# Performance work log

Hardware: AMD Instinct MI355X
Metric: run time of the kernel (lower is better)

Reference implementation:

```python
import jax, jax.numpy as jnp
import numpy as np

# ---- CRF hyperparameters (init_kwargs) ----
NUM_CLASSES = 4
RADIUS = 10            # guided filter radius -> 21x21 kernel
EPS = 1e-4
THETA_GAMMA = 2.5
G_RADIUS = int(THETA_GAMMA * 4)  # gaussian layer radius = 10 -> 21x21 kernel
SPATIAL_COMPAT = 3.0
BILATERAL_COMPAT = 10.0
NUM_ITERATIONS = 5
RGB_W = np.array([0.2989, 0.5870, 0.1140], dtype=np.float32)  # tf rgb_to_grayscale


def _make_kernel(radius, theta):
    x, y = np.mgrid[-radius:radius + 1, -radius:radius + 1]
    k = np.exp(-(x ** 2 + y ** 2) / (2.0 * theta ** 2))
    k = k / k.sum()
    k[radius, radius] = 0.0  # zero out center (no self-message)
    return jnp.asarray(k, dtype=jnp.float32)

_GAUSS_K = _make_kernel(G_RADIUS, THETA_GAMMA)          # spatial gaussian kernel
_GUIDED_K = _make_kernel(RADIUS, RADIUS / 3.0)          # guided-filter gaussian kernel


def _depthwise(src, k2d, r):
    # src: [B,H,W,C], k2d: [kh,kw]; zero-padded depthwise conv (same as pad+VALID)
    c = src.shape[-1]
    kh, kw = k2d.shape
    k = jnp.broadcast_to(k2d[:, :, None, None], (kh, kw, 1, c))
    return jax.lax.conv_general_dilated(
        src, k, window_strides=(1, 1), padding=[(r, r), (r, r)],
        dimension_numbers=('NHWC', 'HWIO', 'NHWC'), feature_group_count=c)


def _gaussian(src):
    return _depthwise(src, _GAUSS_K, G_RADIUS)


def _guided(gray, p):
    # guided gaussian filter with single-channel guide `gray` [B,H,W,1]
    gf = lambda s: _depthwise(s, _GUIDED_K, RADIUS)
    mean_I = gf(gray)                       # [B,H,W,1]
    mean_p = gf(p)                          # [B,H,W,C]
    mean_Ip = gf(gray * p)
    cov_Ip = mean_Ip - mean_I * mean_p
    mean_II = gf(gray * gray)
    var_I = mean_II - mean_I * mean_I
    a = cov_Ip / (var_I + EPS)
    b = mean_p - a * mean_I
    return gf(a) * gray + gf(b)


def setup_inputs() -> dict:
    key = jax.random.key(0)
    k1, k2 = jax.random.split(key)
    unary = jax.random.normal(k1, (1, 512, 512, NUM_CLASSES), dtype=jnp.float32)
    image = jax.random.uniform(k2, (1, 512, 512, 3), dtype=jnp.float32)
    return {"unary": unary, "image": image}


def reference(unary, image):
    gray = (image @ jnp.asarray(RGB_W))[..., None]        # [B,H,W,1]
    ones = jnp.ones_like(unary)
    spatial_norm = _gaussian(ones)
    bilateral_norm = _guided(gray, ones)

    Q = jax.nn.softmax(-unary, axis=-1)
    for _ in range(NUM_ITERATIONS):
        spatial_out = _gaussian(Q) / spatial_norm
        bilateral_out = _guided(gray, Q) / bilateral_norm
        # spatial_weights = SPATIAL_COMPAT*I, bilateral_weights = BILATERAL_COMPAT*I,
        # compatibility = -I  => matmuls reduce to scalar scaling + negation
        message = SPATIAL_COMPAT * spatial_out + BILATERAL_COMPAT * bilateral_out
        pairwise = -message
        Q = jax.nn.softmax(-unary - pairwise, axis=-1)
    return Q
```

## Files before the change

### kernel.cpp

```cpp
#include <hip/hip_runtime.h>
#include <hip/hip_cooperative_groups.h>
#include <hip/hip_fp16.h>
#include <math.h>

namespace cg = cooperative_groups;

#define W 512
#define H 512
#define NPIX (W*H)
#define RAD 10
#define KS 21
#define CRF_EPS 1e-4f

#define TX 32
#define TY 8
#define CIN (TX + 2*RAD)
#define RIN (TY + 2*RAD)
#define GX (W / TX)
#define GY (H / TY)
#define NBLK (GX*GY)
#define NVT (CIN * 4)

#define SM_BYTES 29952
#define OFF_R1 23296

struct W21 { float w[KS]; };

struct Params {
    const float4* unary;
    const float*  image;
    unsigned short* grayh;
    ushort4* Qh;
    float2*  a1b1;
    ushort4* ah;
    ushort4* bh;
    float4*  Qfinal;
    W21 wg, wu;
    float c0g, c0u;
};

__device__ __forceinline__ float4 f4(float x, float y, float z, float w_) {
    return make_float4(x, y, z, w_);
}
__device__ __forceinline__ float4 fma4(float s, float4 a, float4 acc) {
    acc.x = fmaf(s, a.x, acc.x); acc.y = fmaf(s, a.y, acc.y);
    acc.z = fmaf(s, a.z, acc.z); acc.w = fmaf(s, a.w, acc.w);
    return acc;
}
__device__ __forceinline__ int swz(int b, int N) {
    return (b & 7) * (N >> 3) + (b >> 3);
}
__device__ __forceinline__ ushort4 pack4(float4 v) {
    ushort4 r;
    r.x = __half_as_ushort(__float2half_rn(v.x));
    r.y = __half_as_ushort(__float2half_rn(v.y));
    r.z = __half_as_ushort(__float2half_rn(v.z));
    r.w = __half_as_ushort(__float2half_rn(v.w));
    return r;
}
__device__ __forceinline__ float4 unpack4(ushort4 v) {
    return f4(__half2float(__ushort_as_half(v.x)),
              __half2float(__ushort_as_half(v.y)),
              __half2float(__ushort_as_half(v.z)),
              __half2float(__ushort_as_half(v.w)));
}
__device__ __forceinline__ unsigned short packh(float v) {
    return __half_as_ushort(__float2half_rn(v));
}
__device__ __forceinline__ float unpackh(unsigned short v) {
    return __half2float(__ushort_as_half(v));
}


__global__ __launch_bounds__(256, 5) void k_crf(Params P) {
    cg::grid_group grid = cg::this_grid();
    __shared__ __align__(16) char smem[SM_BYTES];
    float4* sQ  = (float4*)smem;
    float2* s2t = (float2*)smem;
    float2* ii0 = (float2*)smem;
    float*  sG  = (float*)(smem + OFF_R1);
    float2* ii1 = (float2*)(smem + OFF_R1);
    float4* i0  = (float4*)smem;
    float4* i1  = (float4*)(smem + 6656);
    float4* i2  = (float4*)(smem + OFF_R1);
    float4* ia  = (float4*)(smem + OFF_R1);
    float4* ib  = (float4*)smem;

    int t = threadIdx.x;
    int L = swz(blockIdx.x, NBLK);
    int x0 = (L & (GX - 1)) * TX, y0 = (L >> 4) * TY;
    int row = t >> 5, col = t & 31;
    int py = y0 + row, px = x0 + col;
    int p = py * W + px;
    int vc = t % CIN, vr0 = (t / CIN) * 2;
    int cidx = (row + RAD) * CIN + col + RAD;

    {
        int pi = blockIdx.x * 256 + t;
        float r = P.image[3 * pi], g = P.image[3 * pi + 1], b = P.image[3 * pi + 2];
        P.grayh[pi] = packh(0.2989f * r + 0.5870f * g + 0.1140f * b);
        float4 u0 = P.unary[pi];
        float mn = fminf(fminf(u0.x, u0.y), fminf(u0.z, u0.w));
        float ex = expf(mn - u0.x), ey = expf(mn - u0.y);
        float ez = expf(mn - u0.z), ew = expf(mn - u0.w);
        float inv = 1.f / (ex + ey + ez + ew);
        P.Qh[pi] = pack4(f4(ex * inv, ey * inv, ez * inv, ew * inv));
    }
    float4 u = P.unary[p];
    float Sgx = 0.f, Sgy = 0.f, Sux = 0.f, Suy = 0.f;
    #pragma unroll
    for (int d = -RAD; d <= RAD; ++d) {
        int xx = px + d, yy = py + d;
        if (xx >= 0 && xx < W) { Sgx += P.wg.w[d + RAD]; Sux += P.wu.w[d + RAD]; }
        if (yy >= 0 && yy < H) { Sgy += P.wg.w[d + RAD]; Suy += P.wu.w[d + RAD]; }
    }
    float s3 = 3.f / (Sgx * Sgy - P.c0g);
    grid.sync();

    for (int i = t; i < RIN * CIN; i += 256) {
        int r = i / CIN, c = i - r * CIN;
        int gx = x0 + c - RAD, gy = y0 + r - RAD;
        float g = 0.f;
        if ((unsigned)gx < W && (unsigned)gy < H) g = unpackh(P.grayh[gy * W + gx]);
        sG[i] = g;
    }
    __syncthreads();
    if (t < NVT) {
        float2 acc0 = make_float2(0.f, 0.f), acc1 = acc0;
        #pragma unroll
        for (int s = 0; s < 22; ++s) {
            float g = sG[(vr0 + s) * CIN + vc];
            if (s <= 20) { float wgv = P.wu.w[s] * g; acc0.x += wgv; acc0.y = fmaf(wgv, g, acc0.y); }
            if (s >= 1)  { float wgv = P.wu.w[s-1] * g; acc1.x += wgv; acc1.y = fmaf(wgv, g, acc1.y); }
        }
        ii0[vr0 * CIN + vc] = acc0;
        ii0[(vr0 + 1) * CIN + vc] = acc1;
    }
    __syncthreads();
    float gv = sG[cidx];
    float mI, iv, ibn;
    {
        float2 A = make_float2(0.f, 0.f);
        #pragma unroll
        for (int d = 0; d < KS; ++d) {
            float2 v = ii0[row * CIN + col + d];
            A.x = fmaf(P.wu.w[d], v.x, A.x);
            A.y = fmaf(P.wu.w[d], v.y, A.y);
        }
        mI = A.x - P.c0u * gv;
        float mII = A.y - P.c0u * gv * gv;
        iv = 1.f / ((mII - mI * mI) + CRF_EPS);
        float N = Sux * Suy - P.c0u;
        float a1v = mI * (1.f - N) * iv;
        float b1v = N - a1v * mI;
        P.a1b1[p] = make_float2(a1v, b1v);
    }
    grid.sync();

    for (int i = t; i < RIN * CIN; i += 256) {
        int r = i / CIN, c = i - r * CIN;
        int gx = x0 + c - RAD, gy = y0 + r - RAD;
        float2 v = make_float2(0.f, 0.f);
        if ((unsigned)gx < W && (unsigned)gy < H) v = P.a1b1[gy * W + gx];
        s2t[i] = v;
    }
    __syncthreads();
    if (t < NVT) {
        float2 acc0 = make_float2(0.f, 0.f), acc1 = acc0;
        #pragma unroll
        for (int s = 0; s < 22; ++s) {
            float2 v = s2t[(vr0 + s) * CIN + vc];
            if (s <= 20) { acc0.x = fmaf(P.wu.w[s], v.x, acc0.x); acc0.y = fmaf(P.wu.w[s], v.y, acc0.y); }
            if (s >= 1)  { acc1.x = fmaf(P.wu.w[s-1], v.x, acc1.x); acc1.y = fmaf(P.wu.w[s-1], v.y, acc1.y); }
        }
        ii1[vr0 * CIN + vc] = acc0;
        ii1[(vr0 + 1) * CIN + vc] = acc1;
    }
    __syncthreads();
    {
        float2 A = make_float2(0.f, 0.f);
        #pragma unroll
        for (int d = 0; d < KS; ++d) {
            float2 v = ii1[row * CIN + col + d];
            A.x = fmaf(P.wu.w[d], v.x, A.x);
            A.y = fmaf(P.wu.w[d], v.y, A.y);
        }
        float2 cen = s2t[cidx];
        float va = A.x - P.c0u * cen.x;
        float vb = A.y - P.c0u * cen.y;
        ibn = 10.f / (va * gv + vb);
    }

    float px_part, py_part, pz_part, pw_part;
    for (int it = 0; it < 5; ++it) {
        __syncthreads();
        for (int i = t; i < RIN * CIN; i += 256) {
            int r = i / CIN, c = i - r * CIN;
            int gx = x0 + c - RAD, gy = y0 + r - RAD;
            float4 q = f4(0.f, 0.f, 0.f, 0.f); float g = 0.f;
            if ((unsigned)gx < W && (unsigned)gy < H) {
                int pp = gy * W + gx;
                q = unpack4(P.Qh[pp]); g = unpackh(P.grayh[pp]);
            }
            sQ[i] = q; sG[i] = g;
        }
        __syncthreads();
        float4 Qc = sQ[cidx];
        float4 a0[2], a1r[2], a2[2];
        if (t < NVT) {
            #pragma unroll
            for (int j = 0; j < 2; ++j) { a0[j] = f4(0,0,0,0); a1r[j] = a0[j]; a2[j] = a0[j]; }
            #pragma unroll
            for (int s = 0; s < 22; ++s) {
                float4 q = sQ[(vr0 + s) * CIN + vc];
                float g = sG[(vr0 + s) * CIN + vc];
                float4 gq = f4(g * q.x, g * q.y, g * q.z, g * q.w);
                if (s <= 20) {
                    a0[0]  = fma4(P.wg.w[s], q, a0[0]);
                    a1r[0] = fma4(P.wu.w[s], q, a1r[0]);
                    a2[0]  = fma4(P.wu.w[s], gq, a2[0]);
                }
                if (s >= 1) {
                    a0[1]  = fma4(P.wg.w[s-1], q, a0[1]);
                    a1r[1] = fma4(P.wu.w[s-1], q, a1r[1]);
                    a2[1]  = fma4(P.wu.w[s-1], gq, a2[1]);
                }
            }
        }
        __syncthreads();
        if (t < NVT) {
            #pragma unroll
            for (int j = 0; j < 2; ++j) {
                i0[(vr0 + j) * CIN + vc] = a0[j];
                i1[(vr0 + j) * CIN + vc] = a1r[j];
                i2[(vr0 + j) * CIN + vc] = a2[j];
            }
        }
        __syncthreads();
        {
            float4 A0 = f4(0,0,0,0), A1 = A0, A2 = A0;
            #pragma unroll
            for (int d = 0; d < KS; ++d) {
                A0 = fma4(P.wg.w[d], i0[row * CIN + col + d], A0);
                A1 = fma4(P.wu.w[d], i1[row * CIN + col + d], A1);
                A2 = fma4(P.wu.w[d], i2[row * CIN + col + d], A2);
            }
            float4 g4  = fma4(-P.c0g, Qc, A0);
            float4 m4  = fma4(-P.c0u, Qc, A1);
            float4 mi4 = fma4(-P.c0u * gv, Qc, A2);
            float4 a, b;
            a.x = (mi4.x - mI * m4.x) * iv; a.y = (mi4.y - mI * m4.y) * iv;
            a.z = (mi4.z - mI * m4.z) * iv; a.w = (mi4.w - mI * m4.w) * iv;
            b.x = m4.x - a.x * mI; b.y = m4.y - a.y * mI;
            b.z = m4.z - a.z * mI; b.w = m4.w - a.w * mI;
            px_part = fmaf(s3, g4.x, -u.x); py_part = fmaf(s3, g4.y, -u.y);
            pz_part = fmaf(s3, g4.z, -u.z); pw_part = fmaf(s3, g4.w, -u.w);
            P.ah[p] = pack4(a); P.bh[p] = pack4(b);
        }
        grid.sync();

        for (int i = t; i < RIN * CIN; i += 256) {
            int r = i / CIN, c = i - r * CIN;
            int gx = x0 + c - RAD, gy = y0 + r - RAD;
            float4 v = f4(0.f, 0.f, 0.f, 0.f);
            if ((unsigned)gx < W && (unsigned)gy < H) v = unpack4(P.ah[gy * W + gx]);
            sQ[i] = v;
        }
        __syncthreads();
        float4 Ac = sQ[cidx];
        if (t < NVT) {
            float4 va0 = f4(0,0,0,0), va1 = va0;
            #pragma unroll
            for (int s = 0; s < 22; ++s) {
                float4 v = sQ[(vr0 + s) * CIN + vc];
                if (s <= 20) va0 = fma4(P.wu.w[s], v, va0);
                if (s >= 1)  va1 = fma4(P.wu.w[s-1], v, va1);
            }
            ia[vr0 * CIN + vc] = va0;
            ia[(vr0 + 1) * CIN + vc] = va1;
        }
        __syncthreads();
        for (int i = t; i < RIN * CIN; i += 256) {
            int r = i / CIN, c = i - r * CIN;
            int gx = x0 + c - RAD, gy = y0 + r - RAD;
            float4 v = f4(0.f, 0.f, 0.f, 0.f);
            if ((unsigned)gx < W && (unsigned)gy < H) v = unpack4(P.bh[gy * W + gx]);
            sQ[i] = v;
        }
        __syncthreads();
        float4 Bc = sQ[cidx];
        float4 vb0 = f4(0,0,0,0), vb1 = vb0;
        if (t < NVT) {
            #pragma unroll
            for (int s = 0; s < 22; ++s) {
                float4 v = sQ[(vr0 + s) * CIN + vc];
                if (s <= 20) vb0 = fma4(P.wu.w[s], v, vb0);
                if (s >= 1)  vb1 = fma4(P.wu.w[s-1], v, vb1);
            }
        }
        __syncthreads();
        if (t < NVT) {
            ib[vr0 * CIN + vc] = vb0;
            ib[(vr0 + 1) * CIN + vc] = vb1;
        }
        __syncthreads();
        {
            float4 VA = f4(0,0,0,0), VB = VA;
            #pragma unroll
            for (int d = 0; d < KS; ++d) {
                VA = fma4(P.wu.w[d], ia[row * CIN + col + d], VA);
                VB = fma4(P.wu.w[d], ib[row * CIN + col + d], VB);
            }
            float4 a4 = fma4(-P.c0u, Ac, VA);
            float4 b4 = fma4(-P.c0u, Bc, VB);
            float lx = fmaf(fmaf(a4.x, gv, b4.x), ibn, px_part);
            float ly = fmaf(fmaf(a4.y, gv, b4.y), ibn, py_part);
            float lz = fmaf(fmaf(a4.z, gv, b4.z), ibn, pz_part);
            float lw = fmaf(fmaf(a4.w, gv, b4.w), ibn, pw_part);
            float m = fmaxf(fmaxf(lx, ly), fmaxf(lz, lw));
            float ex = expf(lx - m), ey = expf(ly - m);
            float ez = expf(lz - m), ew = expf(lw - m);
            float inv = 1.f / (ex + ey + ez + ew);
            float4 qn = f4(ex * inv, ey * inv, ez * inv, ew * inv);
            if (it == 4) P.Qfinal[p] = qn;
            else         P.Qh[p] = pack4(qn);
        }
        if (it < 4) grid.sync();
    }
}


__global__ __launch_bounds__(256) void fb_init(const float* __restrict__ img,
        const float4* __restrict__ unary, unsigned short* __restrict__ grayh,
        ushort4* __restrict__ Qh, float* __restrict__ Sg, float* __restrict__ Su,
        W21 wg, W21 wu) {
    int t = threadIdx.x;
    if (blockIdx.x < 2) {
        int x = blockIdx.x * 256 + t;
        float sg = 0.f, su = 0.f;
        #pragma unroll
        for (int d = -RAD; d <= RAD; ++d) {
            int xx = x + d;
            if (xx >= 0 && xx < W) { sg += wg.w[d + RAD]; su += wu.w[d + RAD]; }
        }
        Sg[x] = sg; Su[x] = su;
    }
    int b = swz(blockIdx.x, NPIX / 256);
    int p = b * 256 + t;
    float r = img[3 * p], g = img[3 * p + 1], bch = img[3 * p + 2];
    grayh[p] = packh(0.2989f * r + 0.5870f * g + 0.1140f * bch);
    float4 u = unary[p];
    float mn = fminf(fminf(u.x, u.y), fminf(u.z, u.w));
    float ex = expf(mn - u.x), ey = expf(mn - u.y), ez = expf(mn - u.z), ew = expf(mn - u.w);
    float inv = 1.f / (ex + ey + ez + ew);
    Qh[p] = pack4(f4(ex * inv, ey * inv, ez * inv, ew * inv));
}

__global__ __launch_bounds__(256, 4) void fb_s1(const unsigned short* __restrict__ grayh,
        const float* __restrict__ Su, float* __restrict__ mean_I,
        float* __restrict__ inv_var, float2* __restrict__ a1b1,
        W21 wu, float c0u) {
    __shared__ float  sg[RIN][CIN];
    __shared__ float2 ii[TY][CIN];
    int L = swz(blockIdx.x, NBLK);
    int x0 = (L & (GX - 1)) * TX, y0 = (L >> 4) * TY;
    int t = threadIdx.x;
    for (int i = t; i < RIN * CIN; i += 256) {
        int r = i / CIN, c = i - r * CIN;
        int gx = x0 + c - RAD, gy = y0 + r - RAD;
        float g = 0.f;
        if ((unsigned)gx < W && (unsigned)gy < H) g = unpackh(grayh[gy * W + gx]);
        sg[r][c] = g;
    }
    __syncthreads();
    if (t < NVT) {
        int c = t % CIN, r0 = (t / CIN) * 2;
        float2 acc0 = make_float2(0.f, 0.f), acc1 = acc0;
        #pragma unroll
        for (int s = 0; s < 22; ++s) {
            float g = sg[r0 + s][c];
            if (s <= 20) { float wgv = wu.w[s] * g; acc0.x += wgv; acc0.y = fmaf(wgv, g, acc0.y); }
            if (s >= 1)  { float wgv = wu.w[s-1] * g; acc1.x += wgv; acc1.y = fmaf(wgv, g, acc1.y); }
        }
        ii[r0][c] = acc0; ii[r0 + 1][c] = acc1;
    }
    __syncthreads();
    int row = t >> 5, col = t & 31;
    float2 A = make_float2(0.f, 0.f);
    #pragma unroll
    for (int d = 0; d < KS; ++d) {
        float2 v = ii[row][col + d];
        A.x = fmaf(wu.w[d], v.x, A.x);
        A.y = fmaf(wu.w[d], v.y, A.y);
    }
    int py = y0 + row, px = x0 + col;
    int p = py * W + px;
    float gc = sg[row + RAD][col + RAD];
    float mI = A.x - c0u * gc;
    float mII = A.y - c0u * gc * gc;
    float iv = 1.f / ((mII - mI * mI) + CRF_EPS);
    float N = Su[px] * Su[py] - c0u;
    float av = mI * (1.f - N) * iv;
    float bv = N - av * mI;
    mean_I[p] = mI; inv_var[p] = iv; a1b1[p] = make_float2(av, bv);
}

__global__ __launch_bounds__(256, 4) void fb_s2(const float2* __restrict__ a1b1,
        const unsigned short* __restrict__ grayh, float* __restrict__ inv_bn,
        W21 wu, float c0u) {
    __shared__ float2 s2[RIN][CIN];
// ... 144 lines not shown
    for (int i = t; i < RIN * CIN; i += 256) {
        int r = i / CIN, c = i - r * CIN;
        int gx = x0 + c - RAD, gy = y0 + r - RAD;
        float4 v = f4(0.f, 0.f, 0.f, 0.f);
        if ((unsigned)gx < W && (unsigned)gy < H) v = unpack4(A[gy * W + gx]);
        sT[i] = v;
    }
    __syncthreads();
    float4 Ac = sT[(row + RAD) * CIN + col + RAD];
    float4 va0 = f4(0,0,0,0), va1 = va0;
    if (t < NVT) {
        #pragma unroll
        for (int s = 0; s < 22; ++s) {
            float4 v = sT[(vr0 + s) * CIN + vc];
            if (s <= 20) va0 = fma4(wu.w[s], v, va0);
            if (s >= 1)  va1 = fma4(wu.w[s-1], v, va1);
        }
        ia[vr0 * CIN + vc] = va0;
        ia[(vr0 + 1) * CIN + vc] = va1;
    }
    __syncthreads();
    for (int i = t; i < RIN * CIN; i += 256) {
        int r = i / CIN, c = i - r * CIN;
        int gx = x0 + c - RAD, gy = y0 + r - RAD;
        float4 v = f4(0.f, 0.f, 0.f, 0.f);
        if ((unsigned)gx < W && (unsigned)gy < H) v = unpack4(B[gy * W + gx]);
        sT[i] = v;
    }
    __syncthreads();
    float4 Bc = sT[(row + RAD) * CIN + col + RAD];
    float4 vb0 = f4(0,0,0,0), vb1 = vb0;
    if (t < NVT) {
        #pragma unroll
        for (int s = 0; s < 22; ++s) {
            float4 v = sT[(vr0 + s) * CIN + vc];
            if (s <= 20) vb0 = fma4(wu.w[s], v, vb0);
            if (s >= 1)  vb1 = fma4(wu.w[s-1], v, vb1);
        }
    }
    __syncthreads();
    if (t < NVT) {
        ib[vr0 * CIN + vc] = vb0;
        ib[(vr0 + 1) * CIN + vc] = vb1;
    }
    __syncthreads();
    float4 VA = f4(0,0,0,0), VB = VA;
    #pragma unroll
    for (int d = 0; d < KS; ++d) {
        VA = fma4(wu.w[d], ia[row * CIN + col + d], VA);
        VB = fma4(wu.w[d], ib[row * CIN + col + d], VB);
    }
    float4 a4 = fma4(-c0u, Ac, VA);
    float4 b4 = fma4(-c0u, Bc, VB);
    float lx = fmaf(fmaf(a4.x, gv, b4.x), ibn, part.x);
    float ly = fmaf(fmaf(a4.y, gv, b4.y), ibn, part.y);
    float lz = fmaf(fmaf(a4.z, gv, b4.z), ibn, part.z);
    float lw = fmaf(fmaf(a4.w, gv, b4.w), ibn, part.w);
    float m = fmaxf(fmaxf(lx, ly), fmaxf(lz, lw));
    float ex = expf(lx - m), ey = expf(ly - m), ez = expf(lz - m), ew = expf(lw - m);
    float inv = 1.f / (ex + ey + ez + ew);
    float4 qn = f4(ex * inv, ey * inv, ez * inv, ew * inv);
    if (last) QoutF[p] = qn;
    else      QoutH[p] = pack4(qn);
}


static void make_w_host(double theta, W21* w, float* c0) {
    double tmp[KS], s = 0.0;
    for (int d = -RAD; d <= RAD; ++d) {
        double v = exp(-(double)(d * d) / (2.0 * theta * theta));
        tmp[d + RAD] = v; s += v;
    }
    for (int i = 0; i < KS; ++i) w->w[i] = (float)(tmp[i] / s);
    *c0 = (float)(1.0 / (s * s));
}

extern "C" void kernel_launch(void* const* d_in, const int* in_sizes, int n_in,
                              void* d_out, int out_size, void* d_ws, size_t ws_size,
                              hipStream_t stream) {
    const float4* unary = (const float4*)d_in[0];
    const float* image = (const float*)d_in[1];
    char* wsb = (char*)d_ws;

    unsigned short* grayh = (unsigned short*)wsb;
    ushort4* Qh      = (ushort4*)(wsb + 524288);
    ushort4* ah      = (ushort4*)(wsb + 2621440);
    ushort4* bh      = (ushort4*)(wsb + 4718592);
    float4*  partial = (float4*)(wsb + 6815744);
    float*   mean_I  = (float*)(wsb + 11010048);
    float*   inv_var = (float*)(wsb + 12058624);
    float*   inv_bn  = (float*)(wsb + 13107200);
    float2*  a1b1    = (float2*)(wsb + 14155776);
    float*   Sg      = (float*)(wsb + 16252928);
    float*   Su      = (float*)(wsb + 16255040);

    W21 wg, wu; float c0g, c0u;
    make_w_host(2.5, &wg, &c0g);
    make_w_host(10.0 / 3.0, &wu, &c0u);

    int dev = 0;
    (void)hipGetDevice(&dev);
    int coop = 0, nCU = 0, blkPerCU = 0;
    (void)hipDeviceGetAttribute(&coop, hipDeviceAttributeCooperativeLaunch, dev);
    (void)hipDeviceGetAttribute(&nCU, hipDeviceAttributeMultiprocessorCount, dev);
    (void)hipOccupancyMaxActiveBlocksPerMultiprocessor(&blkPerCU,
            (const void*)k_crf, 256, 0);
    bool useCoop = (coop != 0) && ((long)blkPerCU * nCU >= NBLK);

    hipError_t st = hipErrorUnknown;
    if (useCoop) {
        Params P;
        P.unary = unary; P.image = image; P.grayh = grayh; P.Qh = Qh;
        P.a1b1 = a1b1; P.ah = ah; P.bh = bh;
        P.Qfinal = (float4*)d_out;
        P.wg = wg; P.wu = wu; P.c0g = c0g; P.c0u = c0u;
        void* args[] = { &P };
        st = hipLaunchCooperativeKernel((const void*)k_crf, dim3(NBLK), dim3(256),
                                        args, 0, stream);
    }
    if (st != hipSuccess) {
        dim3 bl(256), grEl(NPIX / 256), grT(NBLK);
        fb_init<<<grEl, bl, 0, stream>>>(image, unary, grayh, Qh, Sg, Su, wg, wu);
        fb_s1<<<grT, bl, 0, stream>>>(grayh, Su, mean_I, inv_var, a1b1, wu, c0u);
        fb_s2<<<grT, bl, 0, stream>>>(a1b1, grayh, inv_bn, wu, c0u);
        for (int it = 0; it < 5; ++it) {
            fb_f1<<<grT, bl, 0, stream>>>(Qh, grayh, mean_I, inv_var, Sg,
                                          unary, ah, bh, partial, wg, wu, c0g, c0u);
            fb_f2<<<grT, bl, 0, stream>>>(ah, bh, partial, grayh, inv_bn,
                                          (float4*)d_out, Qh, (it == 4) ? 1 : 0,
                                          wu, c0u);
        }
    }
}
```

Before: 171.3 us.

## Keep gray tile resident, store fp16 tiles in LDS, two pixels per thread

Gray is now computed straight from the image into a shared-memory tile that stays resident for every iteration, so the global grayh buffer, its write and the grid sync before its use all go away. Q, a and b tiles are kept as packed fp16 in LDS and unpacked when read, and the horizontal pass has 128 threads each produce two adjacent pixels, sharing loaded taps. The shared-memory layout is rearranged so some syncs merge. Half the threads now sit idle in the horizontal pass, and LDS usage grows slightly, which could reduce occupancy.

Result: no change. 171.7 us (+0.3%).

```diff
diff --git a/kernel.cpp b/kernel.cpp
--- a/kernel.cpp
+++ b/kernel.cpp
@@ -21,15 +21,14 @@
 #define NBLK (GX*GY)
 #define NVT (CIN * 4)
 
-#define SM_BYTES 29952
-#define OFF_R1 23296
+#define SM_BYTES 30784
+#define SG_OFF 24960
 
 struct W21 { float w[KS]; };
 
 struct Params {
     const float4* unary;
     const float*  image;
-    unsigned short* grayh;
     ushort4* Qh;
     float2*  a1b1;
     ushort4* ah;
@@ -75,30 +74,30 @@
 __global__ __launch_bounds__(256, 5) void k_crf(Params P) {
     cg::grid_group grid = cg::this_grid();
     __shared__ __align__(16) char smem[SM_BYTES];
-    float4* sQ  = (float4*)smem;
-    float2* s2t = (float2*)smem;
-    float2* ii0 = (float2*)smem;
-    float*  sG  = (float*)(smem + OFF_R1);
-    float2* ii1 = (float2*)(smem + OFF_R1);
-    float4* i0  = (float4*)smem;
-    float4* i1  = (float4*)(smem + 6656);
-    float4* i2  = (float4*)(smem + OFF_R1);
-    float4* ia  = (float4*)(smem + OFF_R1);
-    float4* ib  = (float4*)smem;
+    ushort4* sQh = (ushort4*)(smem + 13312);
+    float4*  i0  = (float4*)smem;
+    float4*  i1  = (float4*)(smem + 6656);
+    float4*  i2  = (float4*)(smem + 13312);
+    ushort4* sAB = (ushort4*)smem;
+    float4*  ia  = (float4*)(smem + 11648);
+    float4*  ib  = (float4*)(smem + 18304);
+    float2*  s12 = (float2*)smem;
+    float2*  ii1 = (float2*)(smem + 11648);
+    float2*  ii0 = (float2*)smem;
+    float*   sG  = (float*)(smem + SG_OFF);
 
     int t = threadIdx.x;
     int L = swz(blockIdx.x, NBLK);
     int x0 = (L & (GX - 1)) * TX, y0 = (L >> 4) * TY;
-    int row = t >> 5, col = t & 31;
-    int py = y0 + row, px = x0 + col;
-    int p = py * W + px;
+    int hrow = t >> 4, hx = (t & 15) * 2;
+    int py = y0 + hrow, px0 = x0 + hx;
+    int p0 = py * W + px0;
     int vc = t % CIN, vr0 = (t / CIN) * 2;
-    int cidx = (row + RAD) * CIN + col + RAD;
+    int hbase = hrow * CIN + hx;
+    int ccen = (hrow + RAD) * CIN + hx + RAD;
 
     {
         int pi = blockIdx.x * 256 + t;
-        float r = P.image[3 * pi], g = P.image[3 * pi + 1], b = P.image[3 * pi + 2];
-        P.grayh[pi] = packh(0.2989f * r + 0.5870f * g + 0.1140f * b);
         float4 u0 = P.unary[pi];
         float mn = fminf(fminf(u0.x, u0.y), fminf(u0.z, u0.w));
         float ex = expf(mn - u0.x), ey = expf(mn - u0.y);
@@ -106,25 +105,37 @@
         float inv = 1.f / (ex + ey + ez + ew);
         P.Qh[pi] = pack4(f4(ex * inv, ey * inv, ez * inv, ew * inv));
     }
-    float4 u = P.unary[p];
-    float Sgx = 0.f, Sgy = 0.f, Sux = 0.f, Suy = 0.f;
-    #pragma unroll
-    for (int d = -RAD; d <= RAD; ++d) {
-        int xx = px + d, yy = py + d;
-        if (xx >= 0 && xx < W) { Sgx += P.wg.w[d + RAD]; Sux += P.wu.w[d + RAD]; }
-        if (yy >= 0 && yy < H) { Sgy += P.wg.w[d + RAD]; Suy += P.wu.w[d + RAD]; }
-    }
-    float s3 = 3.f / (Sgx * Sgy - P.c0g);
-    grid.sync();
-
     for (int i = t; i < RIN * CIN; i += 256) {
         int r = i / CIN, c = i - r * CIN;
         int gx = x0 + c - RAD, gy = y0 + r - RAD;
         float g = 0.f;
-        if ((unsigned)gx < W && (unsigned)gy < H) g = unpackh(P.grayh[gy * W + gx]);
+        if ((unsigned)gx < W && (unsigned)gy < H) {
+            int pp = gy * W + gx;
+            g = 0.2989f * P.image[3 * pp] + 0.5870f * P.image[3 * pp + 1]
+              + 0.1140f * P.image[3 * pp + 2];
+        }
         sG[i] = g;
     }
     __syncthreads();
+    float gc0 = 0.f, gc1 = 0.f, s3_0 = 0.f, s3_1 = 0.f;
+    float Nu0 = 0.f, Nu1 = 0.f;
+    if (t < 128) {
+        gc0 = sG[ccen]; gc1 = sG[ccen + 1];
+        float Sgx0 = 0.f, Sgx1 = 0.f, Sgy = 0.f;
+        float Sux0 = 0.f, Sux1 = 0.f, Suy = 0.f;
+        #pragma unroll
+        for (int d = -RAD; d <= RAD; ++d) {
+            int xa = px0 + d, xb = px0 + 1 + d, yy = py + d;
+            float wgd = P.wg.w[d + RAD], wud = P.wu.w[d + RAD];
+            if (xa >= 0 && xa < W) { Sgx0 += wgd; Sux0 += wud; }
+            if (xb >= 0 && xb < W) { Sgx1 += wgd; Sux1 += wud; }
+            if (yy >= 0 && yy < H) { Sgy  += wgd; Suy  += wud; }
+        }
+        s3_0 = 3.f / (Sgx0 * Sgy - P.c0g);
+        s3_1 = 3.f / (Sgx1 * Sgy - P.c0g);
+        Nu0 = Sux0 * Suy - P.c0u;
+        Nu1 = Sux1 * Suy - P.c0u;
+    }
     if (t < NVT) {
         float2 acc0 = make_float2(0.f, 0.f), acc1 = acc0;
         #pragma unroll
@@ -137,23 +148,25 @@
         ii0[(vr0 + 1) * CIN + vc] = acc1;
     }
     __syncthreads();
-    float gv = sG[cidx];
-    float mI, iv, ibn;
-    {
-        float2 A = make_float2(0.f, 0.f);
-        #pragma unroll
-        for (int d = 0; d < KS; ++d) {
-            float2 v = ii0[row * CIN + col + d];
-            A.x = fmaf(P.wu.w[d], v.x, A.x);
-            A.y = fmaf(P.wu.w[d], v.y, A.y);
-        }
-        mI = A.x - P.c0u * gv;
-        float mII = A.y - P.c0u * gv * gv;
-        iv = 1.f / ((mII - mI * mI) + CRF_EPS);
-        float N = Sux * Suy - P.c0u;
-        float a1v = mI * (1.f - N) * iv;
-        float b1v = N - a1v * mI;
-        P.a1b1[p] = make_float2(a1v, b1v);
+    float mI0 = 0.f, mI1 = 0.f, iv0 = 0.f, iv1 = 0.f, ibn0 = 0.f, ibn1 = 0.f;
+    if (t < 128) {
+        float2 A0 = make_float2(0.f, 0.f), A1 = A0;
+        #pragma unroll
+        for (int d = 0; d < 22; ++d) {
+            float2 v = ii0[hbase + d];
+            if (d <= 20) { A0.x = fmaf(P.wu.w[d], v.x, A0.x); A0.y = fmaf(P.wu.w[d], v.y, A0.y); }
+            if (d >= 1)  { A1.x = fmaf(P.wu.w[d-1], v.x, A1.x); A1.y = fmaf(P.wu.w[d-1], v.y, A1.y); }
+        }
+        mI0 = A0.x - P.c0u * gc0;
+        float mII0 = A0.y - P.c0u * gc0 * gc0;
+        iv0 = 1.f / ((mII0 - mI0 * mI0) + CRF_EPS);
+        float a1v0 = mI0 * (1.f - Nu0) * iv0;
+        P.a1b1[p0] = make_float2(a1v0, Nu0 - a1v0 * mI0);
+        mI1 = A1.x - P.c0u * gc1;
+        float mII1 = A1.y - P.c0u * gc1 * gc1;
+        iv1 = 1.f / ((mII1 - mI1 * mI1) + CRF_EPS);
+        float a1v1 = mI1 * (1.f - Nu1) * iv1;
+        P.a1b1[p0 + 1] = make_float2(a1v1, Nu1 - a1v1 * mI1);
     }
     grid.sync();
 
@@ -162,14 +175,14 @@
         int gx = x0 + c - RAD, gy = y0 + r - RAD;
         float2 v = make_float2(0.f, 0.f);
         if ((unsigned)gx < W && (unsigned)gy < H) v = P.a1b1[gy * W + gx];
-        s2t[i] = v;
+        s12[i] = v;
     }
     __syncthreads();
     if (t < NVT) {
         float2 acc0 = make_float2(0.f, 0.f), acc1 = acc0;
         #pragma unroll
         for (int s = 0; s < 22; ++s) {
-            float2 v = s2t[(vr0 + s) * CIN + vc];
+            float2 v = s12[(vr0 + s) * CIN + vc];
             if (s <= 20) { acc0.x = fmaf(P.wu.w[s], v.x, acc0.x); acc0.y = fmaf(P.wu.w[s], v.y, acc0.y); }
             if (s >= 1)  { acc1.x = fmaf(P.wu.w[s-1], v.x, acc1.x); acc1.y = fmaf(P.wu.w[s-1], v.y, acc1.y); }
         }
@@ -177,102 +190,120 @@
         ii1[(vr0 + 1) * CIN + vc] = acc1;
     }
     __syncthreads();
-    {
-        float2 A = make_float2(0.f, 0.f);
-        #pragma unroll
-        for (int d = 0; d < KS; ++d) {
-            float2 v = ii1[row * CIN + col + d];
-            A.x = fmaf(P.wu.w[d], v.x, A.x);
-            A.y = fmaf(P.wu.w[d], v.y, A.y);
-        }
-        float2 cen = s2t[cidx];
-        float va = A.x - P.c0u * cen.x;
-        float vb = A.y - P.c0u * cen.y;
-        ibn = 10.f / (va * gv + vb);
-    }
-
-    float px_part, py_part, pz_part, pw_part;
+    if (t < 128) {
+        float2 A0 = make_float2(0.f, 0.f), A1 = A0;
+        #pragma unroll
+        for (int d = 0; d < 22; ++d) {
+            float2 v = ii1[hbase + d];
+            if (d <= 20) { A0.x = fmaf(P.wu.w[d], v.x, A0.x); A0.y = fmaf(P.wu.w[d], v.y, A0.y); }
+            if (d >= 1)  { A1.x = fmaf(P.wu.w[d-1], v.x, A1.x); A1.y = fmaf(P.wu.w[d-1], v.y, A1.y); }
+        }
+        float2 c0 = s12[ccen], c1 = s12[ccen + 1];
+        ibn0 = 10.f / ((A0.x - P.c0u * c0.x) * gc0 + (A0.y - P.c0u * c0.y));
+        ibn1 = 10.f / ((A1.x - P.c0u * c1.x) * gc1 + (A1.y - P.c0u * c1.y));
+    }
+
+    float4 part0, part1;
     for (int it = 0; it < 5; ++it) {
         __syncthreads();
         for (int i = t; i < RIN * CIN; i += 256) {
             int r = i / CIN, c = i - r * CIN;
             int gx = x0 + c - RAD, gy = y0 + r - RAD;
-            float4 q = f4(0.f, 0.f, 0.f, 0.f); float g = 0.f;
-            if ((unsigned)gx < W && (unsigned)gy < H) {
-                int pp = gy * W + gx;
-                q = unpack4(P.Qh[pp]); g = unpackh(P.grayh[pp]);
-            }
-            sQ[i] = q; sG[i] = g;
+            ushort4 q = make_ushort4(0, 0, 0, 0);
+            if ((unsigned)gx < W && (unsigned)gy < H) q = P.Qh[gy * W + gx];
+            sQh[i] = q;
         }
         __syncthreads();
-        float4 Qc = sQ[cidx];
-        float4 a0[2], a1r[2], a2[2];
+        float4 Qc0, Qc1;
+        if (t < 128) { Qc0 = unpack4(sQh[ccen]); Qc1 = unpack4(sQh[ccen + 1]); }
+        float4 a2h[2];
         if (t < NVT) {
-            #pragma unroll
-            for (int j = 0; j < 2; ++j) { a0[j] = f4(0,0,0,0); a1r[j] = a0[j]; a2[j] = a0[j]; }
+            float4 a0[2], a1r[2];
+            #pragma unroll
+            for (int j = 0; j < 2; ++j) { a0[j] = f4(0,0,0,0); a1r[j] = a0[j]; a2h[j] = a0[j]; }
             #pragma unroll
             for (int s = 0; s < 22; ++s) {
-                float4 q = sQ[(vr0 + s) * CIN + vc];
+                float4 q = unpack4(sQh[(vr0 + s) * CIN + vc]);
                 float g = sG[(vr0 + s) * CIN + vc];
                 float4 gq = f4(g * q.x, g * q.y, g * q.z, g * q.w);
                 if (s <= 20) {
                     a0[0]  = fma4(P.wg.w[s], q, a0[0]);
                     a1r[0] = fma4(P.wu.w[s], q, a1r[0]);
-                    a2[0]  = fma4(P.wu.w[s], gq, a2[0]);
+                    a2h[0] = fma4(P.wu.w[s], gq, a2h[0]);
                 }
                 if (s >= 1) {
                     a0[1]  = fma4(P.wg.w[s-1], q, a0[1]);
                     a1r[1] = fma4(P.wu.w[s-1], q, a1r[1]);
-                    a2[1]  = fma4(P.wu.w[s-1], gq, a2[1]);
+                    a2h[1] = fma4(P.wu.w[s-1], gq, a2h[1]);
                 }
             }
+            i0[vr0 * CIN + vc] = a0[0];
+            i0[(vr0 + 1) * CIN + vc] = a0[1];
+            i1[vr0 * CIN + vc] = a1r[0];
+            i1[(vr0 + 1) * CIN + vc] = a1r[1];
         }
         __syncthreads();
         if (t < NVT) {
+            i2[vr0 * CIN + vc] = a2h[0];
+            i2[(vr0 + 1) * CIN + vc] = a2h[1];
+        }
+        __syncthreads();
+        if (t < 128) {
+            float4 A0[2], A1[2], A2[2];
+            #pragma unroll
+            for (int j = 0; j < 2; ++j) { A0[j] = f4(0,0,0,0); A1[j] = A0[j]; A2[j] = A0[j]; }
+            #pragma unroll
+            for (int d = 0; d < 22; ++d) {
+                float4 v0 = i0[hbase + d], v1 = i1[hbase + d], v2 = i2[hbase + d];
+                if (d <= 20) {
+                    A0[0] = fma4(P.wg.w[d], v0, A0[0]);
+                    A1[0] = fma4(P.wu.w[d], v1, A1[0]);
+                    A2[0] = fma4(P.wu.w[d], v2, A2[0]);
+                }
+                if (d >= 1) {
+                    A0[1] = fma4(P.wg.w[d-1], v0, A0[1]);
+                    A1[1] = fma4(P.wu.w[d-1], v1, A1[1]);
+                    A2[1] = fma4(P.wu.w[d-1], v2, A2[1]);
+                }
+            }
             #pragma unroll
             for (int j = 0; j < 2; ++j) {
-                i0[(vr0 + j) * CIN + vc] = a0[j];
-                i1[(vr0 + j) * CIN + vc] = a1r[j];
-                i2[(vr0 + j) * CIN + vc] = a2[j];
-            }
-        }
-        __syncthreads();
-        {
-            float4 A0 = f4(0,0,0,0), A1 = A0, A2 = A0;
-            #pragma unroll
-            for (int d = 0; d < KS; ++d) {
-                A0 = fma4(P.wg.w[d], i0[row * CIN + col + d], A0);
-                A1 = fma4(P.wu.w[d], i1[row * CIN + col + d], A1);
-                A2 = fma4(P.wu.w[d], i2[row * CIN + col + d], A2);
-            }
-            float4 g4  = fma4(-P.c0g, Qc, A0);
-            float4 m4  = fma4(-P.c0u, Qc, A1);
-            float4 mi4 = fma4(-P.c0u * gv, Qc, A2);
-            float4 a, b;
-            a.x = (mi4.x - mI * m4.x) * iv; a.y = (mi4.y - mI * m4.y) * iv;
-            a.z = (mi4.z - mI * m4.z) * iv; a.w = (mi4.w - mI * m4.w) * iv;
-            b.x = m4.x - a.x * mI; b.y = m4.y - a.y * mI;
-            b.z = m4.z - a.z * mI; b.w = m4.w - a.w * mI;
-            px_part = fmaf(s3, g4.x, -u.x); py_part = fmaf(s3, g4.y, -u.y);
-            pz_part = fmaf(s3, g4.z, -u.z); pw_part = fmaf(s3, g4.w, -u.w);
-            P.ah[p] = pack4(a); P.bh[p] = pack4(b);
+                float4 Qc = j ? Qc1 : Qc0;
+                float gcj = j ? gc1 : gc0;
+                float mIj = j ? mI1 : mI0, ivj = j ? iv1 : iv0;
+                float s3j = j ? s3_1 : s3_0;
+                float4 g4  = fma4(-P.c0g, Qc, A0[j]);
+                float4 m4  = fma4(-P.c0u, Qc, A1[j]);
+                float4 mi4 = fma4(-P.c0u * gcj, Qc, A2[j]);
+                float4 a, b;
+                a.x = (mi4.x - mIj * m4.x) * ivj; a.y = (mi4.y - mIj * m4.y) * ivj;
+                a.z = (mi4.z - mIj * m4.z) * ivj; a.w = (mi4.w - mIj * m4.w) * ivj;
+                b.x = m4.x - a.x * mIj; b.y = m4.y - a.y * mIj;
+                b.z = m4.z - a.z * mIj; b.w = m4.w - a.w * mIj;
+                float4 u = P.unary[p0 + j];
+                float4 pt = f4(fmaf(s3j, g4.x, -u.x), fmaf(s3j, g4.y, -u.y),
+                               fmaf(s3j, g4.z, -u.z), fmaf(s3j, g4.w, -u.w));
+                if (j) part1 = pt; else part0 = pt;
+                P.ah[p0 + j] = pack4(a); P.bh[p0 + j] = pack4(b);
+            }
         }
         grid.sync();
 
         for (int i = t; i < RIN * CIN; i += 256) {
             int r = i / CIN, c = i - r * CIN;
             int gx = x0 + c - RAD, gy = y0 + r - RAD;
-            float4 v = f4(0.f, 0.f, 0.f, 0.f);
-            if ((unsigned)gx < W && (unsigned)gy < H) v = unpack4(P.ah[gy * W + gx]);
-            sQ[i] = v;
+            ushort4 v = make_ushort4(0, 0, 0, 0);
+            if ((unsigned)gx < W && (unsigned)gy < H) v = P.ah[gy * W + gx];
+            sAB[i] = v;
         }
         __syncthreads();
-        float4 Ac = sQ[cidx];
+        float4 Ac0, Ac1;
+        if (t < 128) { Ac0 = unpack4(sAB[ccen]); Ac1 = unpack4(sAB[ccen + 1]); }
         if (t < NVT) {
             float4 va0 = f4(0,0,0,0), va1 = va0;
             #pragma unroll
             for (int s = 0; s < 22; ++s) {
-                float4 v = sQ[(vr0 + s) * CIN + vc];
+                float4 v = unpack4(sAB[(vr0 + s) * CIN + vc]);
                 if (s <= 20) va0 = fma4(P.wu.w[s], v, va0);
                 if (s >= 1)  va1 = fma4(P.wu.w[s-1], v, va1);
             }
@@ -283,47 +314,54 @@
         for (int i = t; i < RIN * CIN; i += 256) {
             int r = i / CIN, c = i - r * CIN;
             int gx = x0 + c - RAD, gy = y0 + r - RAD;
-            float4 v = f4(0.f, 0.f, 0.f, 0.f);
-            if ((unsigned)gx < W && (unsigned)gy < H) v = unpack4(P.bh[gy * W + gx]);
-            sQ[i] = v;
+            ushort4 v = make_ushort4(0, 0, 0, 0);
+            if ((unsigned)gx < W && (unsigned)gy < H) v = P.bh[gy * W + gx];
+            sAB[i] = v;
         }
         __syncthreads();
-        float4 Bc = sQ[cidx];
-        float4 vb0 = f4(0,0,0,0), vb1 = vb0;
+        float4 Bc0, Bc1;
+        if (t < 128) { Bc0 = unpack4(sAB[ccen]); Bc1 = unpack4(sAB[ccen + 1]); }
         if (t < NVT) {
+            float4 vb0 = f4(0,0,0,0), vb1 = vb0;
             #pragma unroll
             for (int s = 0; s < 22; ++s) {
-                float4 v = sQ[(vr0 + s) * CIN + vc];
+                float4 v = unpack4(sAB[(vr0 + s) * CIN + vc]);
                 if (s <= 20) vb0 = fma4(P.wu.w[s], v, vb0);
                 if (s >= 1)  vb1 = fma4(P.wu.w[s-1], v, vb1);
             }
-        }
-        __syncthreads();
-        if (t < NVT) {
             ib[vr0 * CIN + vc] = vb0;
             ib[(vr0 + 1) * CIN + vc] = vb1;
         }
         __syncthreads();
-        {
-            float4 VA = f4(0,0,0,0), VB = VA;
-            #pragma unroll
-            for (int d = 0; d < KS; ++d) {
-                VA = fma4(P.wu.w[d], ia[row * CIN + col + d], VA);
-                VB = fma4(P.wu.w[d], ib[row * CIN + col + d], VB);
-            }
-            float4 a4 = fma4(-P.c0u, Ac, VA);
-            float4 b4 = fma4(-P.c0u, Bc, VB);
-            float lx = fmaf(fmaf(a4.x, gv, b4.x), ibn, px_part);
-            float ly = fmaf(fmaf(a4.y, gv, b4.y), ibn, py_part);
-            float lz = fmaf(fmaf(a4.z, gv, b4.z), ibn, pz_part);
-            float lw = fmaf(fmaf(a4.w, gv, b4.w), ibn, pw_part);
-            float m = fmaxf(fmaxf(lx, ly), fmaxf(lz, lw));
-            float ex = expf(lx - m), ey = expf(ly - m);
-            float ez = expf(lz - m), ew = expf(lw - m);
-            float inv = 1.f / (ex + ey + ez + ew);
-            float4 qn = f4(ex * inv, ey * inv, ez * inv, ew * inv);
-            if (it == 4) P.Qfinal[p] = qn;
-            else         P.Qh[p] = pack4(qn);
+        if (t < 128) {
+            float4 VA[2], VB[2];
+            #pragma unroll
+            for (int j = 0; j < 2; ++j) { VA[j] = f4(0,0,0,0); VB[j] = VA[j]; }
+            #pragma unroll
+            for (int d = 0; d < 22; ++d) {
+                float4 va = ia[hbase + d], vb = ib[hbase + d];
+                if (d <= 20) { VA[0] = fma4(P.wu.w[d], va, VA[0]); VB[0] = fma4(P.wu.w[d], vb, VB[0]); }
+                if (d >= 1)  { VA[1] = fma4(P.wu.w[d-1], va, VA[1]); VB[1] = fma4(P.wu.w[d-1], vb, VB[1]); }
+            }
+            #pragma unroll
+            for (int j = 0; j < 2; ++j) {
+                float4 Ac = j ? Ac1 : Ac0, Bc = j ? Bc1 : Bc0;
+                float gcj = j ? gc1 : gc0, ibnj = j ? ibn1 : ibn0;
+                float4 pt = j ? part1 : part0;
+                float4 a4 = fma4(-P.c0u, Ac, VA[j]);
+                float4 b4 = fma4(-P.c0u, Bc, VB[j]);
+                float lx = fmaf(fmaf(a4.x, gcj, b4.x), ibnj, pt.x);
+                float ly = fmaf(fmaf(a4.y, gcj, b4.y), ibnj, pt.y);
+                float lz = fmaf(fmaf(a4.z, gcj, b4.z), ibnj, pt.z);
+                float lw = fmaf(fmaf(a4.w, gcj, b4.w), ibnj, pt.w);
+                float m = fmaxf(fmaxf(lx, ly), fmaxf(lz, lw));
+                float ex = expf(lx - m), ey = expf(ly - m);
+                float ez = expf(lz - m), ew = expf(lw - m);
+                float inv = 1.f / (ex + ey + ez + ew);
+                float4 qn = f4(ex * inv, ey * inv, ez * inv, ew * inv);
+                if (it == 4) P.Qfinal[p0 + j] = qn;
+                else         P.Qh[p0 + j] = pack4(qn);
+            }
         }
         if (it < 4) grid.sync();
     }
@@ -664,7 +702,7 @@
     hipError_t st = hipErrorUnknown;
     if (useCoop) {
         Params P;
-        P.unary = unary; P.image = image; P.grayh = grayh; P.Qh = Qh;
+        P.unary = unary; P.image = image; P.Qh = Qh;
         P.a1b1 = a1b1; P.ah = ah; P.bh = bh;
         P.Qfinal = (float4*)d_out;
         P.wg = wg; P.wu = wu; P.c0g = c0g; P.c0u = c0u;
```

## Replace per-iteration grid syncs with neighbor-tile flag waits and double buffers

Applied to the files above, without the earlier changes.

Each tile now publishes per-tile progress flags and waits only on the up to 15 neighboring tiles whose halo it reads, instead of a full grid.sync twice per iteration. Q, a and b are double-buffered by iteration parity so faster tiles cannot overwrite data a slow neighbor still needs. The first-pass accumulator stores are also split so the a2 stores go after a barrier, which frees smem regions earlier. This aims to cut global barrier latency and load imbalance, at the cost of atomic spin-waits, extra fences, and more workspace.

Result: no change. 170.7 us (-0.3%).

```diff
diff --git a/kernel.cpp b/kernel.cpp
--- a/kernel.cpp
+++ b/kernel.cpp
@@ -30,11 +30,12 @@
     const float4* unary;
     const float*  image;
     unsigned short* grayh;
-    ushort4* Qh;
+    ushort4* qA; ushort4* qB;
     float2*  a1b1;
-    ushort4* ah;
-    ushort4* bh;
+    ushort4* aA; ushort4* aB;
+    ushort4* bA; ushort4* bB;
     float4*  Qfinal;
+    int* flag_q; int* flag_ab;
     W21 wg, wu;
     float c0g, c0u;
 };
@@ -69,6 +70,11 @@
 }
 __device__ __forceinline__ float unpackh(unsigned short v) {
     return __half2float(__ushort_as_half(v));
+}
+
+__device__ __forceinline__ void spin_ge(const int* f, int v) {
+    while (__hip_atomic_load(f, __ATOMIC_RELAXED, __HIP_MEMORY_SCOPE_AGENT) < v)
+        __builtin_amdgcn_s_sleep(2);
 }
 
 
@@ -88,12 +94,22 @@
 
     int t = threadIdx.x;
     int L = swz(blockIdx.x, NBLK);
-    int x0 = (L & (GX - 1)) * TX, y0 = (L >> 4) * TY;
+    int txi = L & (GX - 1), tyi = L >> 4;
+    int x0 = txi * TX, y0 = tyi * TY;
     int row = t >> 5, col = t & 31;
     int py = y0 + row, px = x0 + col;
     int p = py * W + px;
     int vc = t % CIN, vr0 = (t / CIN) * 2;
     int cidx = (row + RAD) * CIN + col + RAD;
+
+    int nbL = 0;
+    if (t < 15) {
+        int dy = t / 3 - 2, dx = t % 3 - 1;
+        int ty2 = tyi + dy; ty2 = ty2 < 0 ? 0 : (ty2 > GY - 1 ? GY - 1 : ty2);
+        int tx2 = txi + dx; tx2 = tx2 < 0 ? 0 : (tx2 > GX - 1 ? GX - 1 : tx2);
+        nbL = ty2 * GX + tx2;
+    }
+    if (t == 0) { P.flag_q[L] = 0; P.flag_ab[L] = 0; }
 
     {
         int pi = blockIdx.x * 256 + t;
@@ -104,7 +120,7 @@
         float ex = expf(mn - u0.x), ey = expf(mn - u0.y);
         float ez = expf(mn - u0.z), ew = expf(mn - u0.w);
         float inv = 1.f / (ex + ey + ez + ew);
-        P.Qh[pi] = pack4(f4(ex * inv, ey * inv, ez * inv, ew * inv));
+        P.qA[pi] = pack4(f4(ex * inv, ey * inv, ez * inv, ew * inv));
     }
     float4 u = P.unary[p];
     float Sgx = 0.f, Sgy = 0.f, Sux = 0.f, Suy = 0.f;
@@ -116,6 +132,8 @@
     }
     float s3 = 3.f / (Sgx * Sgy - P.c0g);
     grid.sync();
+    if (t == 0)
+        __hip_atomic_store(&P.flag_q[L], 1, __ATOMIC_RELAXED, __HIP_MEMORY_SCOPE_AGENT);
 
     for (int i = t; i < RIN * CIN; i += 256) {
         int r = i / CIN, c = i - r * CIN;
@@ -193,23 +211,31 @@
 
     float px_part, py_part, pz_part, pw_part;
     for (int it = 0; it < 5; ++it) {
-        __syncthreads();
+        const ushort4* qin  = (it & 1) ? P.qB : P.qA;
+        ushort4*       qout = (it & 1) ? P.qA : P.qB;
+        ushort4*       aw   = (it & 1) ? P.aB : P.aA;
+        ushort4*       bw   = (it & 1) ? P.bB : P.bA;
+
+        if (t < 15) spin_ge(&P.flag_q[nbL], it + 1);
+        __syncthreads();
+        __threadfence();
         for (int i = t; i < RIN * CIN; i += 256) {
             int r = i / CIN, c = i - r * CIN;
             int gx = x0 + c - RAD, gy = y0 + r - RAD;
             float4 q = f4(0.f, 0.f, 0.f, 0.f); float g = 0.f;
             if ((unsigned)gx < W && (unsigned)gy < H) {
                 int pp = gy * W + gx;
-                q = unpack4(P.Qh[pp]); g = unpackh(P.grayh[pp]);
+                q = unpack4(qin[pp]); g = unpackh(P.grayh[pp]);
             }
             sQ[i] = q; sG[i] = g;
         }
         __syncthreads();
         float4 Qc = sQ[cidx];
-        float4 a0[2], a1r[2], a2[2];
+        float4 a2h[2];
         if (t < NVT) {
+            float4 a0[2], a1r[2];
             #pragma unroll
-            for (int j = 0; j < 2; ++j) { a0[j] = f4(0,0,0,0); a1r[j] = a0[j]; a2[j] = a0[j]; }
+            for (int j = 0; j < 2; ++j) { a0[j] = f4(0,0,0,0); a1r[j] = a0[j]; a2h[j] = a0[j]; }
             #pragma unroll
             for (int s = 0; s < 22; ++s) {
                 float4 q = sQ[(vr0 + s) * CIN + vc];
@@ -218,25 +244,27 @@
                 if (s <= 20) {
                     a0[0]  = fma4(P.wg.w[s], q, a0[0]);
                     a1r[0] = fma4(P.wu.w[s], q, a1r[0]);
-                    a2[0]  = fma4(P.wu.w[s], gq, a2[0]);
+                    a2h[0] = fma4(P.wu.w[s], gq, a2h[0]);
                 }
                 if (s >= 1) {
                     a0[1]  = fma4(P.wg.w[s-1], q, a0[1]);
                     a1r[1] = fma4(P.wu.w[s-1], q, a1r[1]);
-                    a2[1]  = fma4(P.wu.w[s-1], gq, a2[1]);
+                    a2h[1] = fma4(P.wu.w[s-1], gq, a2h[1]);
                 }
             }
+            i0[vr0 * CIN + vc] = a0[0];
+            i0[(vr0 + 1) * CIN + vc] = a0[1];
+            i1[vr0 * CIN + vc] = a1r[0];
+            i1[(vr0 + 1) * CIN + vc] = a1r[1];
         }
         __syncthreads();
         if (t < NVT) {
-            #pragma unroll
-            for (int j = 0; j < 2; ++j) {
-                i0[(vr0 + j) * CIN + vc] = a0[j];
-                i1[(vr0 + j) * CIN + vc] = a1r[j];
-                i2[(vr0 + j) * CIN + vc] = a2[j];
-            }
-        }
-        __syncthreads();
+            i2[vr0 * CIN + vc] = a2h[0];
+            i2[(vr0 + 1) * CIN + vc] = a2h[1];
+        }
+        __syncthreads();
+        if (t < 128) {
+        }
         {
             float4 A0 = f4(0,0,0,0), A1 = A0, A2 = A0;
             #pragma unroll
@@ -255,15 +283,22 @@
             b.z = m4.z - a.z * mI; b.w = m4.w - a.w * mI;
             px_part = fmaf(s3, g4.x, -u.x); py_part = fmaf(s3, g4.y, -u.y);
             pz_part = fmaf(s3, g4.z, -u.z); pw_part = fmaf(s3, g4.w, -u.w);
-            P.ah[p] = pack4(a); P.bh[p] = pack4(b);
-        }
-        grid.sync();
-
+            aw[p] = pack4(a); bw[p] = pack4(b);
+        }
+        __threadfence();
+        __syncthreads();
+        if (t == 0)
+            __hip_atomic_store(&P.flag_ab[L], it + 1, __ATOMIC_RELEASE,
+                               __HIP_MEMORY_SCOPE_AGENT);
+
+        if (t < 15) spin_ge(&P.flag_ab[nbL], it + 1);
+        __syncthreads();
+        __threadfence();
         for (int i = t; i < RIN * CIN; i += 256) {
             int r = i / CIN, c = i - r * CIN;
             int gx = x0 + c - RAD, gy = y0 + r - RAD;
             float4 v = f4(0.f, 0.f, 0.f, 0.f);
-            if ((unsigned)gx < W && (unsigned)gy < H) v = unpack4(P.ah[gy * W + gx]);
+            if ((unsigned)gx < W && (unsigned)gy < H) v = unpack4(aw[gy * W + gx]);
             sQ[i] = v;
         }
         __syncthreads();
@@ -284,7 +319,7 @@
             int r = i / CIN, c = i - r * CIN;
             int gx = x0 + c - RAD, gy = y0 + r - RAD;
             float4 v = f4(0.f, 0.f, 0.f, 0.f);
-            if ((unsigned)gx < W && (unsigned)gy < H) v = unpack4(P.bh[gy * W + gx]);
+            if ((unsigned)gx < W && (unsigned)gy < H) v = unpack4(bw[gy * W + gx]);
             sQ[i] = v;
         }
         __syncthreads();
@@ -323,9 +358,15 @@
             float inv = 1.f / (ex + ey + ez + ew);
             float4 qn = f4(ex * inv, ey * inv, ez * inv, ew * inv);
             if (it == 4) P.Qfinal[p] = qn;
-            else         P.Qh[p] = pack4(qn);
-        }
-        if (it < 4) grid.sync();
+            else         qout[p] = pack4(qn);
+        }
+        if (it < 4) {
+            __threadfence();
+            __syncthreads();
+            if (t == 0)
+                __hip_atomic_store(&P.flag_q[L], it + 2, __ATOMIC_RELEASE,
+                                   __HIP_MEMORY_SCOPE_AGENT);
+        }
     }
 }
 
@@ -636,17 +677,22 @@
     const float* image = (const float*)d_in[1];
     char* wsb = (char*)d_ws;
 
-    unsigned short* grayh = (unsigned short*)wsb;
-    ushort4* Qh      = (ushort4*)(wsb + 524288);
-    ushort4* ah      = (ushort4*)(wsb + 2621440);
-    ushort4* bh      = (ushort4*)(wsb + 4718592);
-    float4*  partial = (float4*)(wsb + 6815744);
-    float*   mean_I  = (float*)(wsb + 11010048);
-    float*   inv_var = (float*)(wsb + 12058624);
-    float*   inv_bn  = (float*)(wsb + 13107200);
-    float2*  a1b1    = (float2*)(wsb + 14155776);
-    float*   Sg      = (float*)(wsb + 16252928);
-    float*   Su      = (float*)(wsb + 16255040);
+    ushort4* qA      = (ushort4*)wsb;
+    ushort4* qB      = (ushort4*)(wsb + 2097152);
+    ushort4* aA      = (ushort4*)(wsb + 4194304);
+    ushort4* aB      = (ushort4*)(wsb + 6291456);
+    ushort4* bA      = (ushort4*)(wsb + 8388608);
+    ushort4* bB      = (ushort4*)(wsb + 10485760);
+    unsigned short* grayh = (unsigned short*)(wsb + 12582912);
+    float2*  a1b1    = (float2*)(wsb + 13107200);
+    float4*  partial = (float4*)(wsb + 15204352);
+    float*   mean_I  = (float*)(wsb + 19398656);
+    float*   inv_var = (float*)(wsb + 20447232);
+    float*   inv_bn  = (float*)(wsb + 21495808);
+    float*   Sg      = (float*)(wsb + 22544384);
+    float*   Su      = (float*)(wsb + 22546432);
+    int*     flag_q  = (int*)(wsb + 22548480);
+    int*     flag_ab = (int*)(wsb + 22552576);
 
     W21 wg, wu; float c0g, c0u;
     make_w_host(2.5, &wg, &c0g);
@@ -664,9 +710,11 @@
     hipError_t st = hipErrorUnknown;
     if (useCoop) {
         Params P;
-        P.unary = unary; P.image = image; P.grayh = grayh; P.Qh = Qh;
-        P.a1b1 = a1b1; P.ah = ah; P.bh = bh;
+        P.unary = unary; P.image = image; P.grayh = grayh;
+        P.qA = qA; P.qB = qB; P.a1b1 = a1b1;
+        P.aA = aA; P.aB = aB; P.bA = bA; P.bB = bB;
         P.Qfinal = (float4*)d_out;
+        P.flag_q = flag_q; P.flag_ab = flag_ab;
         P.wg = wg; P.wu = wu; P.c0g = c0g; P.c0u = c0u;
         void* args[] = { &P };
         st = hipLaunchCooperativeKernel((const void*)k_crf, dim3(NBLK), dim3(256),
@@ -674,14 +722,14 @@
     }
     if (st != hipSuccess) {
         dim3 bl(256), grEl(NPIX / 256), grT(NBLK);
-        fb_init<<<grEl, bl, 0, stream>>>(image, unary, grayh, Qh, Sg, Su, wg, wu);
+        fb_init<<<grEl, bl, 0, stream>>>(image, unary, grayh, qA, Sg, Su, wg, wu);
         fb_s1<<<grT, bl, 0, stream>>>(grayh, Su, mean_I, inv_var, a1b1, wu, c0u);
         fb_s2<<<grT, bl, 0, stream>>>(a1b1, grayh, inv_bn, wu, c0u);
         for (int it = 0; it < 5; ++it) {
-            fb_f1<<<grT, bl, 0, stream>>>(Qh, grayh, mean_I, inv_var, Sg,
-                                          unary, ah, bh, partial, wg, wu, c0g, c0u);
-            fb_f2<<<grT, bl, 0, stream>>>(ah, bh, partial, grayh, inv_bn,
-                                          (float4*)d_out, Qh, (it == 4) ? 1 : 0,
+            fb_f1<<<grT, bl, 0, stream>>>(qA, grayh, mean_I, inv_var, Sg,
+                                          unary, aA, bA, partial, wg, wu, c0g, c0u);
+            fb_f2<<<grT, bl, 0, stream>>>(aA, bA, partial, grayh, inv_bn,
+                                          (float4*)d_out, qA, (it == 4) ? 1 : 0,
                                           wu, c0u);
         }
     }
```
